# Performance work log

Hardware: AMD Instinct MI355X
Metric: run time of the kernel (lower is better)

Reference implementation:

```python
import jax, jax.numpy as jnp
import numpy as np

N_QUBITS = 12
N_LAYERS = 3
N_LABELS = 28
LN_EPS = 1e-5

_CNOT = jnp.array([[1, 0, 0, 0],
                   [0, 1, 0, 0],
                   [0, 0, 0, 1],
                   [0, 0, 1, 0]], dtype=jnp.complex64).reshape(2, 2, 2, 2)


def _apply_1q(state, U, wire):
    # state: (2,)*N_QUBITS complex, U: (2,2)
    state = jnp.tensordot(U, state, axes=((1,), (wire,)))
    return jnp.moveaxis(state, 0, wire)


def _apply_cnot(state, ctrl, tgt):
    state = jnp.tensordot(_CNOT, state, axes=((2, 3), (ctrl, tgt)))
    return jnp.moveaxis(state, (0, 1), (ctrl, tgt))


def _ry(theta):
    c = jnp.cos(theta / 2).astype(jnp.complex64)
    s = jnp.sin(theta / 2).astype(jnp.complex64)
    return jnp.array([[c, -s], [s, c]])


def _rot(phi, theta, omega):
    # PennyLane Rot(phi, theta, omega) = RZ(omega) RY(theta) RZ(phi)
    c = jnp.cos(theta / 2)
    s = jnp.sin(theta / 2)
    ep = jnp.exp(-0.5j * (phi + omega))
    em = jnp.exp(-0.5j * (phi - omega))
    return jnp.array([[ep * c, -jnp.conj(em) * s],
                      [em * s, jnp.conj(ep) * c]]).astype(jnp.complex64)


def _circuit(angles, weights):
    # angles: (N_QUBITS,), weights: (N_LAYERS, N_QUBITS, 3)
    state = jnp.zeros((2,) * N_QUBITS, dtype=jnp.complex64)
    state = state.at[(0,) * N_QUBITS].set(1.0)
    # AngleEmbedding, rotation='Y'
    for w in range(N_QUBITS):
        state = _apply_1q(state, _ry(angles[w]), w)
    # StronglyEntanglingLayers: Rot on each wire then CNOT ring with range r
    for l in range(N_LAYERS):
        for w in range(N_QUBITS):
            state = _apply_1q(state, _rot(weights[l, w, 0], weights[l, w, 1], weights[l, w, 2]), w)
        r = (l % (N_QUBITS - 1)) + 1
        for w in range(N_QUBITS):
            state = _apply_cnot(state, w, (w + r) % N_QUBITS)
    probs = jnp.real(state * jnp.conj(state))
    zs = []
    for w in range(N_QUBITS):
        p = jnp.sum(probs, axis=tuple(i for i in range(N_QUBITS) if i != w))
        zs.append(p[0] - p[1])
    return jnp.stack(zs)


def setup_inputs() -> dict:
    key = jax.random.key(0)
    ks = jax.random.split(key, 10)
    B = 512
    d_in = 768
    return {
        "x": jax.random.normal(ks[0], (B, d_in), dtype=jnp.float32),
        "proj_w": jax.random.normal(ks[1], (N_QUBITS, d_in), dtype=jnp.float32) * (1.0 / np.sqrt(d_in)),
        "proj_b": jnp.zeros((N_QUBITS,), dtype=jnp.float32),
        "ln_w": jnp.ones((N_QUBITS,), dtype=jnp.float32),
        "ln_b": jnp.zeros((N_QUBITS,), dtype=jnp.float32),
        "q_w": jax.random.uniform(ks[2], (N_LAYERS, N_QUBITS, 3), dtype=jnp.float32) * 2 * np.pi,
        "h1_w": jax.random.normal(ks[3], (256, N_QUBITS), dtype=jnp.float32) * (1.0 / np.sqrt(N_QUBITS)),
        "h1_b": jnp.zeros((256,), dtype=jnp.float32),
        "h2_w": jax.random.normal(ks[4], (N_LABELS, 256), dtype=jnp.float32) * (1.0 / np.sqrt(256)),
        "h2_b": jnp.zeros((N_LABELS,), dtype=jnp.float32),
    }


def reference(x, proj_w, proj_b, ln_w, ln_b, q_w, h1_w, h1_b, h2_w, h2_b):
    h = jnp.tanh(x @ proj_w.T + proj_b)                       # (B, 12)
    mu = jnp.mean(h, axis=-1, keepdims=True)
    var = jnp.mean((h - mu) ** 2, axis=-1, keepdims=True)
    hn = (h - mu) / jnp.sqrt(var + LN_EPS) * ln_w + ln_b      # LayerNorm(12)
    q = jax.vmap(_circuit, in_axes=(0, None))(hn, q_w)        # (B, 12) PauliZ expvals
    z = jax.nn.relu(q @ h1_w.T + h1_b)                        # Dropout is identity in eval
    return z @ h2_w.T + h2_b                                  # (B, 28)
```

## Files before the change

kernel.cpp:

```cpp
#include <hip/hip_runtime.h>
#include <math.h>

#define D_IN 768
#define NLAB 28

struct Map { int rb[2]; int lb[6]; int wb[4]; };
constexpr Map MP[4] = {
    {{10, 11}, {4, 5, 6, 7, 8, 9}, {0, 1, 2, 3}},
    {{0, 1}, {2, 3, 8, 9, 10, 11}, {4, 5, 6, 7}},
    {{6, 7}, {5, 4, 2, 3, 0, 1}, {8, 9, 10, 11}},
    {{0, 1}, {2, 3, 8, 9, 10, 11}, {4, 5, 6, 7}},
};
constexpr int regPos(int e, int b) { for (int k = 0; k < 2; ++k) if (MP[e].rb[k] == b) return k; return -1; }
constexpr int lanePos(int e, int b) { for (int j = 0; j < 6; ++j) if (MP[e].lb[j] == b) return j; return -1; }
constexpr int wavePos(int e, int b) { for (int m = 0; m < 4; ++m) if (MP[e].wb[m] == b) return m; return -1; }

constexpr int stateOf(int e, int wv, int lane, int r) {
    int i = 0;
    for (int k = 0; k < 2; ++k) i |= ((r >> k) & 1) << MP[e].rb[k];
    for (int j = 0; j < 6; ++j) i |= ((lane >> j) & 1) << MP[e].lb[j];
    for (int m = 0; m < 4; ++m) i |= ((wv >> m) & 1) << MP[e].wb[m];
    return i;
}
constexpr int slotOf(int e, int i) {
    int r = 0, ln = 0, wv = 0;
    for (int k = 0; k < 2; ++k) r |= ((i >> MP[e].rb[k]) & 1) << k;
    for (int j = 0; j < 6; ++j) ln |= ((i >> MP[e].lb[j]) & 1) << j;
    for (int m = 0; m < 4; ++m) wv |= ((i >> MP[e].wb[m]) & 1) << m;
    return (wv << 8) | (ln << 2) | r;
}
constexpr int swzl(int s) { return s ^ (((s >> 4) ^ (s >> 8)) & 15); }

template <int J>
__device__ __forceinline__ float lx(float v) {
    if constexpr (J == 0 || J == 1 || J == 3) {
        constexpr int ctrl = (J == 0) ? 0xB1 : (J == 1) ? 0x4E : 0x128;
        return __int_as_float(__builtin_amdgcn_update_dpp(
            0, __float_as_int(v), ctrl, 0xF, 0xF, true));
    } else if constexpr (J == 2 || J == 4) {
        constexpr int off = (J == 2) ? 0x101F : 0x401F;
        return __int_as_float(__builtin_amdgcn_ds_swizzle(__float_as_int(v), off));
    } else {
        return __shfl_xor(v, 32, 64);
    }
}
__device__ __forceinline__ float waveRed(float v) {
    v += lx<0>(v); v += lx<1>(v); v += lx<2>(v);
    v += lx<3>(v); v += lx<4>(v); v += lx<5>(v);
    return v;
}

struct CU2 { float2 rr, im; };
struct G4 { CU2 u00, u01, u10, u11; };

__device__ __forceinline__ float2 cmul(const CU2 u, const float2 a) {
    float2 t;
    asm("v_pk_mul_f32 %0, %1, %2 op_sel:[0,1] op_sel_hi:[1,0]"
        : "=v"(t) : "v"(u.im), "v"(a));
    asm("v_pk_fma_f32 %0, %1, %2, %3"
        : "=v"(t) : "v"(u.rr), "v"(a), "v"(t));
    return t;
}
__device__ __forceinline__ float2 cfma(const CU2 u, const float2 a, float2 acc) {
    asm("v_pk_fma_f32 %0, %1, %2, %3 op_sel:[0,1,0] op_sel_hi:[1,0,1]"
        : "=v"(acc) : "v"(u.im), "v"(a), "v"(acc));
    asm("v_pk_fma_f32 %0, %1, %2, %3"
        : "=v"(acc) : "v"(u.rr), "v"(a), "v"(acc));
    return acc;
}

template <int E, int B>
__device__ __forceinline__ void rotg(float2 (&a)[4], int lane, const G4& gg) {
    const G4 g = gg;
    constexpr int k = regPos(E, B);
    if constexpr (k >= 0) {
        constexpr int m = 1 << k;
#pragma unroll
        for (int r = 0; r < 4; ++r)
            if (!(r & m)) {
                const float2 a0 = a[r], a1 = a[r | m];
                a[r]     = cfma(g.u01, a1, cmul(g.u00, a0));
                a[r | m] = cfma(g.u10, a0, cmul(g.u11, a1));
            }
    } else {
        constexpr int j = lanePos(E, B);
        static_assert(j >= 0, "rot on wave bit");
        const bool hi = (lane >> j) & 1;
        CU2 co, cp;
        co.rr = hi ? g.u11.rr : g.u00.rr;  co.im = hi ? g.u11.im : g.u00.im;
        cp.rr = hi ? g.u10.rr : g.u01.rr;  cp.im = hi ? g.u10.im : g.u01.im;
#pragma unroll
        for (int r = 0; r < 4; ++r) {
            float2 p;
            p.x = lx<j>(a[r].x);
            p.y = lx<j>(a[r].y);
            a[r] = cfma(cp, p, cmul(co, a[r]));
        }
    }
}

template <int E, int C, int T>
__device__ __forceinline__ void cnot(float2 (&a)[4], int lane, int wv) {
    constexpr int kc = regPos(E, C), jc = lanePos(E, C), mc = wavePos(E, C);
    constexpr int kt = regPos(E, T), jt = lanePos(E, T);
    static_assert(wavePos(E, T) < 0, "cnot target on wave bit");
    if constexpr (kt >= 0) {
        constexpr int mt = 1 << kt;
        if constexpr (kc >= 0) {
            constexpr int mcb = 1 << kc;
#pragma unroll
            for (int r = 0; r < 4; ++r)
                if ((r & mcb) && !(r & mt)) { float2 t = a[r]; a[r] = a[r | mt]; a[r | mt] = t; }
        } else if constexpr (jc >= 0) {
            const bool p = (lane >> jc) & 1;
#pragma unroll
            for (int r = 0; r < 4; ++r)
                if (!(r & mt)) {
                    const float2 lo = a[r], hi = a[r | mt];
                    a[r].x = p ? hi.x : lo.x;       a[r].y = p ? hi.y : lo.y;
                    a[r | mt].x = p ? lo.x : hi.x;  a[r | mt].y = p ? lo.y : hi.y;
                }
        } else {
            if ((wv >> mc) & 1) {
#pragma unroll
                for (int r = 0; r < 4; ++r)
                    if (!(r & mt)) { float2 t = a[r]; a[r] = a[r | mt]; a[r | mt] = t; }
            }
        }
    } else {
        if constexpr (kc >= 0) {
            constexpr int mcb = 1 << kc;
#pragma unroll
            for (int r = 0; r < 4; ++r)
                if (r & mcb) { a[r].x = lx<jt>(a[r].x); a[r].y = lx<jt>(a[r].y); }
        } else if constexpr (jc >= 0) {
            const bool p = (lane >> jc) & 1;
#pragma unroll
            for (int r = 0; r < 4; ++r) {
                const float px = lx<jt>(a[r].x), py = lx<jt>(a[r].y);
                a[r].x = p ? px : a[r].x;  a[r].y = p ? py : a[r].y;
            }
        } else {
            if ((wv >> mc) & 1) {
#pragma unroll
                for (int r = 0; r < 4; ++r) { a[r].x = lx<jt>(a[r].x); a[r].y = lx<jt>(a[r].y); }
            }
        }
    }
}

template <int PE, int CE>
__device__ __forceinline__ void remap(float2 (&a)[4], int lane, int wv, float2* st) {
    const int wbase = swzl((wv << 8) | (lane << 2));
#pragma unroll
    for (int r = 0; r < 4; ++r) st[wbase ^ r] = a[r];
    __syncthreads();
    const int rbase = swzl(slotOf(PE, stateOf(CE, wv, lane, 0)));
#pragma unroll
    for (int r = 0; r < 4; ++r) {
        const int d = swzl(slotOf(PE, stateOf(CE, 0, 0, r)));
        a[r] = st[rbase ^ d];
    }
    __syncthreads();
}

constexpr int MASKW[12] = {0x124, 0x092, 0x049, 0x900, 0x480, 0x240,
                           0x920, 0x490, 0x248, 0x924, 0x492, 0x249};
constexpr int rmOf(int w) { int v = 0; for (int k = 0; k < 2; ++k) v |= ((MASKW[w] >> MP[3].rb[k]) & 1) << k; return v; }
constexpr int lmOf(int w) { int v = 0; for (int j = 0; j < 6; ++j) v |= ((MASKW[w] >> MP[3].lb[j]) & 1) << j; return v; }
constexpr int wmOf(int w) { int v = 0; for (int m = 0; m < 4; ++m) v |= ((MASKW[w] >> MP[3].wb[m]) & 1) << m; return v; }
constexpr int RMa[12] = {rmOf(0),rmOf(1),rmOf(2),rmOf(3),rmOf(4),rmOf(5),rmOf(6),rmOf(7),rmOf(8),rmOf(9),rmOf(10),rmOf(11)};
constexpr int LMa[12] = {lmOf(0),lmOf(1),lmOf(2),lmOf(3),lmOf(4),lmOf(5),lmOf(6),lmOf(7),lmOf(8),lmOf(9),lmOf(10),lmOf(11)};
constexpr int WMa[12] = {wmOf(0),wmOf(1),wmOf(2),wmOf(3),wmOf(4),wmOf(5),wmOf(6),wmOf(7),wmOf(8),wmOf(9),wmOf(10),wmOf(11)};

__global__ __launch_bounds__(1024, 8) void hybrid_r6(
    const float* __restrict__ x, const float* __restrict__ proj_w,
    const float* __restrict__ proj_b, const float* __restrict__ ln_w,
    const float* __restrict__ ln_b, const float* __restrict__ q_w,
    const float* __restrict__ h1_w, const float* __restrict__ h1_b,
    const float* __restrict__ h2_w, const float* __restrict__ h2_b,
    float* __restrict__ out) {
    __shared__ float2 st[4096];
    __shared__ G4 rotU[36];
    __shared__ float hbuf[12];
    __shared__ float red[12 * 16];
    __shared__ float z1[256];
    __shared__ float qz[12];

    const int b = blockIdx.x;
    const int tid = threadIdx.x;
    const int lane = tid & 63;
    const int wv = tid >> 6;

    if (wv < 12) {
        const float* xr = x + (size_t)b * D_IN;
        const float* wr = proj_w + wv * D_IN;
        float s = 0.f;
#pragma unroll
        for (int k = 0; k < 12; ++k) s += xr[lane + k * 64] * wr[lane + k * 64];
        s = waveRed(s);
        if (lane == 0) hbuf[wv] = tanhf(s + proj_b[wv]);
    }
    __syncthreads();

    if (tid < 36) {
        const float phi = q_w[3 * tid], th = q_w[3 * tid + 1], om = q_w[3 * tid + 2];
        float sth, cth, sa, ca, sb, cb;
        sincosf(0.5f * th, &sth, &cth);
        sincosf(0.5f * (phi + om), &sa, &ca);
        sincosf(0.5f * (phi - om), &sb, &cb);
        float R0r = cth * ca, R0i = -cth * sa;
        float R1r = -sth * cb, R1i = -sth * sb;
        float R2r = sth * cb, R2i = -sth * sb;
        float R3r = cth * ca, R3i = cth * sa;
        if (tid < 12) {
            float mu = 0.f;
#pragma unroll
            for (int k = 0; k < 12; ++k) mu += hbuf[k];
            mu *= (1.f / 12.f);
            float var = 0.f;
#pragma unroll
            for (int k = 0; k < 12; ++k) { const float d = hbuf[k] - mu; var += d * d; }
            var *= (1.f / 12.f);
            const float inv = 1.f / sqrtf(var + 1e-5f);
            const float ang = (hbuf[tid] - mu) * inv * ln_w[tid] + ln_b[tid];
            float sy, cy;
            sincosf(0.5f * ang, &sy, &cy);
            const float M0r = R0r * cy + R1r * sy, M0i = R0i * cy + R1i * sy;
            const float M1r = -R0r * sy + R1r * cy, M1i = -R0i * sy + R1i * cy;
            const float M2r = R2r * cy + R3r * sy, M2i = R2i * cy + R3i * sy;
            const float M3r = -R2r * sy + R3r * cy, M3i = -R2i * sy + R3i * cy;
            R0r = M0r; R0i = M0i; R1r = M1r; R1i = M1i;
            R2r = M2r; R2i = M2i; R3r = M3r; R3i = M3i;
        }
        G4 g;
        g.u00.rr = make_float2(R0r, R0r); g.u00.im = make_float2(-R0i, R0i);
        g.u01.rr = make_float2(R1r, R1r); g.u01.im = make_float2(-R1i, R1i);
        g.u10.rr = make_float2(R2r, R2r); g.u10.im = make_float2(-R2i, R2i);
        g.u11.rr = make_float2(R3r, R3r); g.u11.im = make_float2(-R3i, R3i);
        rotU[tid] = g;
    }
    __syncthreads();

    float2 a[4];
#pragma unroll
    for (int r = 0; r < 4; ++r) a[r] = make_float2(0.f, 0.f);
    if (tid == 0) a[0].x = 1.f;

    rotg<0, 11>(a, lane, rotU[0]); rotg<0, 10>(a, lane, rotU[1]); rotg<0, 9>(a, lane, rotU[2]);
    rotg<0, 8>(a, lane, rotU[3]);  rotg<0, 7>(a, lane, rotU[4]);  rotg<0, 6>(a, lane, rotU[5]);
    rotg<0, 5>(a, lane, rotU[6]);  rotg<0, 4>(a, lane, rotU[7]);
    cnot<0, 11, 10>(a, lane, wv); cnot<0, 10, 9>(a, lane, wv); cnot<0, 9, 8>(a, lane, wv);
    cnot<0, 8, 7>(a, lane, wv);   cnot<0, 7, 6>(a, lane, wv);  cnot<0, 6, 5>(a, lane, wv);
    cnot<0, 5, 4>(a, lane, wv);
    remap<0, 1>(a, lane, wv, st);
    rotg<1, 3>(a, lane, rotU[8]); rotg<1, 2>(a, lane, rotU[9]);
    rotg<1, 1>(a, lane, rotU[10]); rotg<1, 0>(a, lane, rotU[11]);
    cnot<1, 4, 3>(a, lane, wv); cnot<1, 3, 2>(a, lane, wv); cnot<1, 2, 1>(a, lane, wv);
    cnot<1, 1, 0>(a, lane, wv); cnot<1, 0, 11>(a, lane, wv);
    rotg<1, 11>(a, lane, rotU[12]); rotg<1, 10>(a, lane, rotU[13]);
    rotg<1, 9>(a, lane, rotU[14]);  rotg<1, 8>(a, lane, rotU[15]);
    rotg<1, 3>(a, lane, rotU[20]);  rotg<1, 2>(a, lane, rotU[21]);
    rotg<1, 1>(a, lane, rotU[22]);  rotg<1, 0>(a, lane, rotU[23]);
    cnot<1, 11, 9>(a, lane, wv); cnot<1, 10, 8>(a, lane, wv);
    remap<1, 2>(a, lane, wv, st);
    rotg<2, 7>(a, lane, rotU[16]); rotg<2, 6>(a, lane, rotU[17]);
    rotg<2, 5>(a, lane, rotU[18]); rotg<2, 4>(a, lane, rotU[19]);
    cnot<2, 9, 7>(a, lane, wv); cnot<2, 8, 6>(a, lane, wv); cnot<2, 7, 5>(a, lane, wv);
    cnot<2, 6, 4>(a, lane, wv); cnot<2, 5, 3>(a, lane, wv); cnot<2, 4, 2>(a, lane, wv);
    cnot<2, 3, 1>(a, lane, wv); cnot<2, 2, 0>(a, lane, wv);
    rotg<2, 7>(a, lane, rotU[28]); rotg<2, 6>(a, lane, rotU[29]);
    rotg<2, 5>(a, lane, rotU[30]); rotg<2, 4>(a, lane, rotU[31]);
    rotg<2, 3>(a, lane, rotU[32]); rotg<2, 2>(a, lane, rotU[33]);
    remap<2, 3>(a, lane, wv, st);
    cnot<3, 1, 11>(a, lane, wv); cnot<3, 0, 10>(a, lane, wv);
    rotg<3, 11>(a, lane, rotU[24]); rotg<3, 10>(a, lane, rotU[25]);
    rotg<3, 9>(a, lane, rotU[26]);  rotg<3, 8>(a, lane, rotU[27]);
    rotg<3, 1>(a, lane, rotU[34]);  rotg<3, 0>(a, lane, rotU[35]);

    {
        const float p0 = a[0].x * a[0].x + a[0].y * a[0].y;
        const float p1 = a[1].x * a[1].x + a[1].y * a[1].y;
        const float p2 = a[2].x * a[2].x + a[2].y * a[2].y;
        const float p3 = a[3].x * a[3].x + a[3].y * a[3].y;
        const float s[4] = {p0 + p1 + p2 + p3, p0 - p1 + p2 - p3,
                            p0 + p1 - p2 - p3, p0 - p1 - p2 + p3};
#pragma unroll
        for (int w = 0; w < 12; ++w) {
            const int sgn = (__popc(lane & LMa[w]) + __popc(wv & WMa[w])) & 1;
            float v = sgn ? -s[RMa[w]] : s[RMa[w]];
            v = waveRed(v);
            if (lane == 0) red[w * 16 + wv] = v;
        }
    }
    __syncthreads();
    if (tid < 12) {
        float q = 0.f;
#pragma unroll
        for (int m = 0; m < 16; ++m) q += red[tid * 16 + m];
        qz[tid] = q;
    }
    __syncthreads();

    if (tid < 256) {
        float s = h1_b[tid];
#pragma unroll
        for (int k = 0; k < 12; ++k) s += qz[k] * h1_w[tid * 12 + k];
        z1[tid] = fmaxf(s, 0.f);
    }
    __syncthreads();

    if (wv < 14) {
#pragma unroll
        for (int jj = 0; jj < 2; ++jj) {
            const int j = wv * 2 + jj;
            const float* wr = h2_w + j * 256;
            float s = 0.f;
#pragma unroll
            for (int k = 0; k < 4; ++k) s += z1[lane + k * 64] * wr[lane + k * 64];
            s = waveRed(s);
            if (lane == 0) out[(size_t)b * NLAB + j] = s + h2_b[j];
        }
    }
}

extern "C" void kernel_launch(void* const* d_in, const int* in_sizes, int n_in,
                              void* d_out, int out_size, void* d_ws, size_t ws_size,
                              hipStream_t stream) {
    const float* x      = (const float*)d_in[0];
    const float* proj_w = (const float*)d_in[1];
    const float* proj_b = (const float*)d_in[2];
    const float* ln_w   = (const float*)d_in[3];
    const float* ln_b   = (const float*)d_in[4];
    const float* q_w    = (const float*)d_in[5];
    const float* h1_w   = (const float*)d_in[6];
    const float* h1_b   = (const float*)d_in[7];
    const float* h2_w   = (const float*)d_in[8];
    const float* h2_b   = (const float*)d_in[9];
    float* out = (float*)d_out;

    const int B = in_sizes[0] / D_IN;
    hybrid_r6<<<dim3(B), dim3(1024), 0, stream>>>(x, proj_w, proj_b, ln_w, ln_b,
                                                  q_w, h1_w, h1_b, h2_w, h2_b, out);
}
```

Baseline: 32.93 us.

## Split gate preparation into a separate kernel and read gates as scalar operands

```diff
diff --git a/kernel.cpp b/kernel.cpp
--- a/kernel.cpp
+++ b/kernel.cpp
@@ -53,7 +53,22 @@
 struct CU2 { float2 rr, im; };
 struct G4 { CU2 u00, u01, u10, u11; };
 
-__device__ __forceinline__ float2 cmul(const CU2 u, const float2 a) {
+__device__ __forceinline__ float2 cmuls(const CU2 u, const float2 a) {
+    float2 t;
+    asm("v_pk_mul_f32 %0, %1, %2 op_sel:[0,1] op_sel_hi:[1,0]"
+        : "=v"(t) : "s"(u.im), "v"(a));
+    asm("v_pk_fma_f32 %0, %1, %2, %3"
+        : "=v"(t) : "s"(u.rr), "v"(a), "v"(t));
+    return t;
+}
+__device__ __forceinline__ float2 cfmas(const CU2 u, const float2 a, float2 acc) {
+    asm("v_pk_fma_f32 %0, %1, %2, %3 op_sel:[0,1,0] op_sel_hi:[1,0,1]"
+        : "=v"(acc) : "s"(u.im), "v"(a), "v"(acc));
+    asm("v_pk_fma_f32 %0, %1, %2, %3"
+        : "=v"(acc) : "s"(u.rr), "v"(a), "v"(acc));
+    return acc;
+}
+__device__ __forceinline__ float2 cmulv(const CU2 u, const float2 a) {
     float2 t;
     asm("v_pk_mul_f32 %0, %1, %2 op_sel:[0,1] op_sel_hi:[1,0]"
         : "=v"(t) : "v"(u.im), "v"(a));
@@ -61,7 +76,7 @@
         : "=v"(t) : "v"(u.rr), "v"(a), "v"(t));
     return t;
 }
-__device__ __forceinline__ float2 cfma(const CU2 u, const float2 a, float2 acc) {
+__device__ __forceinline__ float2 cfmav(const CU2 u, const float2 a, float2 acc) {
     asm("v_pk_fma_f32 %0, %1, %2, %3 op_sel:[0,1,0] op_sel_hi:[1,0,1]"
         : "=v"(acc) : "v"(u.im), "v"(a), "v"(acc));
     asm("v_pk_fma_f32 %0, %1, %2, %3"
@@ -70,8 +85,8 @@
 }
 
 template <int E, int B>
-__device__ __forceinline__ void rotg(float2 (&a)[4], int lane, const G4& gg) {
-    const G4 g = gg;
+__device__ __forceinline__ void rotg(float2 (&a)[4], int lane, const G4* __restrict__ gp) {
+    const G4 g = *gp;
     constexpr int k = regPos(E, B);
     if constexpr (k >= 0) {
         constexpr int m = 1 << k;
@@ -79,8 +94,8 @@
         for (int r = 0; r < 4; ++r)
             if (!(r & m)) {
                 const float2 a0 = a[r], a1 = a[r | m];
-                a[r]     = cfma(g.u01, a1, cmul(g.u00, a0));
-                a[r | m] = cfma(g.u10, a0, cmul(g.u11, a1));
+                a[r]     = cfmas(g.u01, a1, cmuls(g.u00, a0));
+                a[r | m] = cfmas(g.u10, a0, cmuls(g.u11, a1));
             }
     } else {
         constexpr int j = lanePos(E, B);
@@ -94,7 +109,7 @@
             float2 p;
             p.x = lx<j>(a[r].x);
             p.y = lx<j>(a[r].y);
-            a[r] = cfma(cp, p, cmul(co, a[r]));
+            a[r] = cfmav(cp, p, cmulv(co, a[r]));
         }
     }
 }
@@ -173,37 +188,36 @@
 constexpr int LMa[12] = {lmOf(0),lmOf(1),lmOf(2),lmOf(3),lmOf(4),lmOf(5),lmOf(6),lmOf(7),lmOf(8),lmOf(9),lmOf(10),lmOf(11)};
 constexpr int WMa[12] = {wmOf(0),wmOf(1),wmOf(2),wmOf(3),wmOf(4),wmOf(5),wmOf(6),wmOf(7),wmOf(8),wmOf(9),wmOf(10),wmOf(11)};
 
-__global__ __launch_bounds__(1024, 8) void hybrid_r6(
+__global__ __launch_bounds__(256) void prep_gates(
     const float* __restrict__ x, const float* __restrict__ proj_w,
     const float* __restrict__ proj_b, const float* __restrict__ ln_w,
     const float* __restrict__ ln_b, const float* __restrict__ q_w,
-    const float* __restrict__ h1_w, const float* __restrict__ h1_b,
-    const float* __restrict__ h2_w, const float* __restrict__ h2_b,
-    float* __restrict__ out) {
-    __shared__ float2 st[4096];
-    __shared__ G4 rotU[36];
+    G4* __restrict__ wsF, G4* __restrict__ wsS) {
     __shared__ float hbuf[12];
-    __shared__ float red[12 * 16];
-    __shared__ float z1[256];
-    __shared__ float qz[12];
-
     const int b = blockIdx.x;
     const int tid = threadIdx.x;
     const int lane = tid & 63;
     const int wv = tid >> 6;
 
-    if (wv < 12) {
+    {
         const float* xr = x + (size_t)b * D_IN;
-        const float* wr = proj_w + wv * D_IN;
-        float s = 0.f;
-#pragma unroll
-        for (int k = 0; k < 12; ++k) s += xr[lane + k * 64] * wr[lane + k * 64];
-        s = waveRed(s);
-        if (lane == 0) hbuf[wv] = tanhf(s + proj_b[wv]);
-    }
-    __syncthreads();
-
-    if (tid < 36) {
+        float xv[12];
+#pragma unroll
+        for (int k = 0; k < 12; ++k) xv[k] = xr[lane + k * 64];
+#pragma unroll
+        for (int jj = 0; jj < 3; ++jj) {
+            const int j = wv * 3 + jj;
+            const float* wr = proj_w + j * D_IN;
+            float s = 0.f;
+#pragma unroll
+            for (int k = 0; k < 12; ++k) s += xv[k] * wr[lane + k * 64];
+            s = waveRed(s);
+            if (lane == 0) hbuf[j] = tanhf(s + proj_b[j]);
+        }
+    }
+    __syncthreads();
+
+    if (tid < 36 && (tid < 12 || b == 0)) {
         const float phi = q_w[3 * tid], th = q_w[3 * tid + 1], om = q_w[3 * tid + 2];
         float sth, cth, sa, ca, sb, cb;
         sincosf(0.5f * th, &sth, &cth);
@@ -238,45 +252,62 @@
         g.u01.rr = make_float2(R1r, R1r); g.u01.im = make_float2(-R1i, R1i);
         g.u10.rr = make_float2(R2r, R2r); g.u10.im = make_float2(-R2i, R2i);
         g.u11.rr = make_float2(R3r, R3r); g.u11.im = make_float2(-R3i, R3i);
-        rotU[tid] = g;
-    }
-    __syncthreads();
+        G4* dst = (tid < 12) ? (wsF + (size_t)b * 12 + tid) : (wsS + (tid - 12));
+        *dst = g;
+    }
+}
+
+__global__ __launch_bounds__(1024, 8) void hybrid_r7(
+    const float* __restrict__ h1_w, const float* __restrict__ h1_b,
+    const float* __restrict__ h2_w, const float* __restrict__ h2_b,
+    const G4* __restrict__ wsF, const G4* __restrict__ wsS,
+    float* __restrict__ out) {
+    __shared__ float2 st[4096];
+    __shared__ float red[12 * 16];
+    __shared__ float z1[256];
+    __shared__ float qz[12];
+
+    const int b = blockIdx.x;
+    const int tid = threadIdx.x;
+    const int lane = tid & 63;
+    const int wv = tid >> 6;
+    const G4* __restrict__ gF = wsF + (size_t)b * 12;
 
     float2 a[4];
 #pragma unroll
     for (int r = 0; r < 4; ++r) a[r] = make_float2(0.f, 0.f);
     if (tid == 0) a[0].x = 1.f;
 
-    rotg<0, 11>(a, lane, rotU[0]); rotg<0, 10>(a, lane, rotU[1]); rotg<0, 9>(a, lane, rotU[2]);
-    rotg<0, 8>(a, lane, rotU[3]);  rotg<0, 7>(a, lane, rotU[4]);  rotg<0, 6>(a, lane, rotU[5]);
-    rotg<0, 5>(a, lane, rotU[6]);  rotg<0, 4>(a, lane, rotU[7]);
+    rotg<0, 11>(a, lane, gF + 0); rotg<0, 10>(a, lane, gF + 1); rotg<0, 9>(a, lane, gF + 2);
+    rotg<0, 8>(a, lane, gF + 3);  rotg<0, 7>(a, lane, gF + 4);  rotg<0, 6>(a, lane, gF + 5);
+    rotg<0, 5>(a, lane, gF + 6);  rotg<0, 4>(a, lane, gF + 7);
     cnot<0, 11, 10>(a, lane, wv); cnot<0, 10, 9>(a, lane, wv); cnot<0, 9, 8>(a, lane, wv);
     cnot<0, 8, 7>(a, lane, wv);   cnot<0, 7, 6>(a, lane, wv);  cnot<0, 6, 5>(a, lane, wv);
     cnot<0, 5, 4>(a, lane, wv);
     remap<0, 1>(a, lane, wv, st);
-    rotg<1, 3>(a, lane, rotU[8]); rotg<1, 2>(a, lane, rotU[9]);
-    rotg<1, 1>(a, lane, rotU[10]); rotg<1, 0>(a, lane, rotU[11]);
+    rotg<1, 3>(a, lane, gF + 8);  rotg<1, 2>(a, lane, gF + 9);
+    rotg<1, 1>(a, lane, gF + 10); rotg<1, 0>(a, lane, gF + 11);
     cnot<1, 4, 3>(a, lane, wv); cnot<1, 3, 2>(a, lane, wv); cnot<1, 2, 1>(a, lane, wv);
     cnot<1, 1, 0>(a, lane, wv); cnot<1, 0, 11>(a, lane, wv);
-    rotg<1, 11>(a, lane, rotU[12]); rotg<1, 10>(a, lane, rotU[13]);
-    rotg<1, 9>(a, lane, rotU[14]);  rotg<1, 8>(a, lane, rotU[15]);
-    rotg<1, 3>(a, lane, rotU[20]);  rotg<1, 2>(a, lane, rotU[21]);
-    rotg<1, 1>(a, lane, rotU[22]);  rotg<1, 0>(a, lane, rotU[23]);
+    rotg<1, 11>(a, lane, wsS + 0); rotg<1, 10>(a, lane, wsS + 1);
+    rotg<1, 9>(a, lane, wsS + 2);  rotg<1, 8>(a, lane, wsS + 3);
+    rotg<1, 3>(a, lane, wsS + 8);  rotg<1, 2>(a, lane, wsS + 9);
+    rotg<1, 1>(a, lane, wsS + 10); rotg<1, 0>(a, lane, wsS + 11);
     cnot<1, 11, 9>(a, lane, wv); cnot<1, 10, 8>(a, lane, wv);
     remap<1, 2>(a, lane, wv, st);
-    rotg<2, 7>(a, lane, rotU[16]); rotg<2, 6>(a, lane, rotU[17]);
-    rotg<2, 5>(a, lane, rotU[18]); rotg<2, 4>(a, lane, rotU[19]);
+    rotg<2, 7>(a, lane, wsS + 4); rotg<2, 6>(a, lane, wsS + 5);
+    rotg<2, 5>(a, lane, wsS + 6); rotg<2, 4>(a, lane, wsS + 7);
     cnot<2, 9, 7>(a, lane, wv); cnot<2, 8, 6>(a, lane, wv); cnot<2, 7, 5>(a, lane, wv);
     cnot<2, 6, 4>(a, lane, wv); cnot<2, 5, 3>(a, lane, wv); cnot<2, 4, 2>(a, lane, wv);
     cnot<2, 3, 1>(a, lane, wv); cnot<2, 2, 0>(a, lane, wv);
-    rotg<2, 7>(a, lane, rotU[28]); rotg<2, 6>(a, lane, rotU[29]);
-    rotg<2, 5>(a, lane, rotU[30]); rotg<2, 4>(a, lane, rotU[31]);
-    rotg<2, 3>(a, lane, rotU[32]); rotg<2, 2>(a, lane, rotU[33]);
+    rotg<2, 7>(a, lane, wsS + 16); rotg<2, 6>(a, lane, wsS + 17);
+    rotg<2, 5>(a, lane, wsS + 18); rotg<2, 4>(a, lane, wsS + 19);
+    rotg<2, 3>(a, lane, wsS + 20); rotg<2, 2>(a, lane, wsS + 21);
     remap<2, 3>(a, lane, wv, st);
     cnot<3, 1, 11>(a, lane, wv); cnot<3, 0, 10>(a, lane, wv);
-    rotg<3, 11>(a, lane, rotU[24]); rotg<3, 10>(a, lane, rotU[25]);
-    rotg<3, 9>(a, lane, rotU[26]);  rotg<3, 8>(a, lane, rotU[27]);
-    rotg<3, 1>(a, lane, rotU[34]);  rotg<3, 0>(a, lane, rotU[35]);
+    rotg<3, 11>(a, lane, wsS + 12); rotg<3, 10>(a, lane, wsS + 13);
+    rotg<3, 9>(a, lane, wsS + 14);  rotg<3, 8>(a, lane, wsS + 15);
+    rotg<3, 1>(a, lane, wsS + 22);  rotg<3, 0>(a, lane, wsS + 23);
 
     {
         const float p0 = a[0].x * a[0].x + a[0].y * a[0].y;
@@ -340,6 +371,11 @@
     float* out = (float*)d_out;
 
     const int B = in_sizes[0] / D_IN;
-    hybrid_r6<<<dim3(B), dim3(1024), 0, stream>>>(x, proj_w, proj_b, ln_w, ln_b,
-                                                  q_w, h1_w, h1_b, h2_w, h2_b, out);
-}
+    G4* wsF = (G4*)d_ws;
+    G4* wsS = wsF + (size_t)B * 12;
+
+    prep_gates<<<dim3(B), dim3(256), 0, stream>>>(x, proj_w, proj_b, ln_w, ln_b,
+                                                  q_w, wsF, wsS);
+    hybrid_r7<<<dim3(B), dim3(1024), 0, stream>>>(h1_w, h1_b, h2_w, h2_b,
+                                                  wsF, wsS, out);
+}
```

After: 37.74 us. +14.6%, slower.

## Double-buffer remap scratch, overlap gate build, swap swizzles for DPP/permlane

Applied to the files above, without the earlier changes.

```diff
diff --git a/kernel.cpp b/kernel.cpp
--- a/kernel.cpp
+++ b/kernel.cpp
@@ -37,11 +37,26 @@
         constexpr int ctrl = (J == 0) ? 0xB1 : (J == 1) ? 0x4E : 0x128;
         return __int_as_float(__builtin_amdgcn_update_dpp(
             0, __float_as_int(v), ctrl, 0xF, 0xF, true));
-    } else if constexpr (J == 2 || J == 4) {
-        constexpr int off = (J == 2) ? 0x101F : 0x401F;
-        return __int_as_float(__builtin_amdgcn_ds_swizzle(__float_as_int(v), off));
+    } else if constexpr (J == 2) {
+        const float tshl = __int_as_float(__builtin_amdgcn_update_dpp(
+            0, __float_as_int(v), 0x104, 0xF, 0xF, true));
+        const float tshr = __int_as_float(__builtin_amdgcn_update_dpp(
+            0, __float_as_int(v), 0x114, 0xF, 0xF, true));
+        return (threadIdx.x & 4) ? tshr : tshl;
+    } else if constexpr (J == 4) {
+#if __has_builtin(__builtin_amdgcn_permlane16_swap)
+        auto pr = __builtin_amdgcn_permlane16_swap(__float_as_int(v), __float_as_int(v), false, false);
+        return (__int_as_float((int)pr[0]) + __int_as_float((int)pr[1])) - v;
+#else
+        return __int_as_float(__builtin_amdgcn_ds_swizzle(__float_as_int(v), 0x401F));
+#endif
     } else {
+#if __has_builtin(__builtin_amdgcn_permlane32_swap)
+        auto pr = __builtin_amdgcn_permlane32_swap(__float_as_int(v), __float_as_int(v), false, false);
+        return (__int_as_float((int)pr[0]) + __int_as_float((int)pr[1])) - v;
+#else
         return __shfl_xor(v, 32, 64);
+#endif
     }
 }
 __device__ __forceinline__ float waveRed(float v) {
@@ -53,7 +68,7 @@
 struct CU2 { float2 rr, im; };
 struct G4 { CU2 u00, u01, u10, u11; };
 
-__device__ __forceinline__ float2 cmul(const CU2 u, const float2 a) {
+__device__ __forceinline__ float2 cmulv(const CU2 u, const float2 a) {
     float2 t;
     asm("v_pk_mul_f32 %0, %1, %2 op_sel:[0,1] op_sel_hi:[1,0]"
         : "=v"(t) : "v"(u.im), "v"(a));
@@ -61,7 +76,7 @@
         : "=v"(t) : "v"(u.rr), "v"(a), "v"(t));
     return t;
 }
-__device__ __forceinline__ float2 cfma(const CU2 u, const float2 a, float2 acc) {
+__device__ __forceinline__ float2 cfmav(const CU2 u, const float2 a, float2 acc) {
     asm("v_pk_fma_f32 %0, %1, %2, %3 op_sel:[0,1,0] op_sel_hi:[1,0,1]"
         : "=v"(acc) : "v"(u.im), "v"(a), "v"(acc));
     asm("v_pk_fma_f32 %0, %1, %2, %3"
@@ -79,8 +94,8 @@
         for (int r = 0; r < 4; ++r)
             if (!(r & m)) {
                 const float2 a0 = a[r], a1 = a[r | m];
-                a[r]     = cfma(g.u01, a1, cmul(g.u00, a0));
-                a[r | m] = cfma(g.u10, a0, cmul(g.u11, a1));
+                a[r]     = cfmav(g.u01, a1, cmulv(g.u00, a0));
+                a[r | m] = cfmav(g.u10, a0, cmulv(g.u11, a1));
             }
     } else {
         constexpr int j = lanePos(E, B);
@@ -94,7 +109,7 @@
             float2 p;
             p.x = lx<j>(a[r].x);
             p.y = lx<j>(a[r].y);
-            a[r] = cfma(cp, p, cmul(co, a[r]));
+            a[r] = cfmav(cp, p, cmulv(co, a[r]));
         }
     }
 }
@@ -161,7 +176,6 @@
         const int d = swzl(slotOf(PE, stateOf(CE, 0, 0, r)));
         a[r] = st[rbase ^ d];
     }
-    __syncthreads();
 }
 
 constexpr int MASKW[12] = {0x124, 0x092, 0x049, 0x900, 0x480, 0x240,
@@ -173,14 +187,34 @@
 constexpr int LMa[12] = {lmOf(0),lmOf(1),lmOf(2),lmOf(3),lmOf(4),lmOf(5),lmOf(6),lmOf(7),lmOf(8),lmOf(9),lmOf(10),lmOf(11)};
 constexpr int WMa[12] = {wmOf(0),wmOf(1),wmOf(2),wmOf(3),wmOf(4),wmOf(5),wmOf(6),wmOf(7),wmOf(8),wmOf(9),wmOf(10),wmOf(11)};
 
-__global__ __launch_bounds__(1024, 8) void hybrid_r6(
+__device__ __forceinline__ void buildRot(int g, const float* __restrict__ q_w, float R[8]) {
+    const float phi = q_w[3 * g], th = q_w[3 * g + 1], om = q_w[3 * g + 2];
+    float sth, cth, sa, ca, sb, cb;
+    sincosf(0.5f * th, &sth, &cth);
+    sincosf(0.5f * (phi + om), &sa, &ca);
+    sincosf(0.5f * (phi - om), &sb, &cb);
+    R[0] = cth * ca;  R[1] = -cth * sa;
+    R[2] = -sth * cb; R[3] = -sth * sb;
+    R[4] = sth * cb;  R[5] = -sth * sb;
+    R[6] = cth * ca;  R[7] = cth * sa;
+}
+__device__ __forceinline__ void storeGate(G4* dst, const float R[8]) {
+    G4 g;
+    g.u00.rr = make_float2(R[0], R[0]); g.u00.im = make_float2(-R[1], R[1]);
+    g.u01.rr = make_float2(R[2], R[2]); g.u01.im = make_float2(-R[3], R[3]);
+    g.u10.rr = make_float2(R[4], R[4]); g.u10.im = make_float2(-R[5], R[5]);
+    g.u11.rr = make_float2(R[6], R[6]); g.u11.im = make_float2(-R[7], R[7]);
+    *dst = g;
+}
+
+__global__ __launch_bounds__(1024, 8) void hybrid_r9(
     const float* __restrict__ x, const float* __restrict__ proj_w,
     const float* __restrict__ proj_b, const float* __restrict__ ln_w,
     const float* __restrict__ ln_b, const float* __restrict__ q_w,
     const float* __restrict__ h1_w, const float* __restrict__ h1_b,
     const float* __restrict__ h2_w, const float* __restrict__ h2_b,
     float* __restrict__ out) {
-    __shared__ float2 st[4096];
+    __shared__ float2 st[2][4096];
     __shared__ G4 rotU[36];
     __shared__ float hbuf[12];
     __shared__ float red[12 * 16];
@@ -201,44 +235,35 @@
         s = waveRed(s);
         if (lane == 0) hbuf[wv] = tanhf(s + proj_b[wv]);
     }
-    __syncthreads();
-
-    if (tid < 36) {
-        const float phi = q_w[3 * tid], th = q_w[3 * tid + 1], om = q_w[3 * tid + 2];
-        float sth, cth, sa, ca, sb, cb;
-        sincosf(0.5f * th, &sth, &cth);
-        sincosf(0.5f * (phi + om), &sa, &ca);
-        sincosf(0.5f * (phi - om), &sb, &cb);
-        float R0r = cth * ca, R0i = -cth * sa;
-        float R1r = -sth * cb, R1i = -sth * sb;
-        float R2r = sth * cb, R2i = -sth * sb;
-        float R3r = cth * ca, R3i = cth * sa;
-        if (tid < 12) {
-            float mu = 0.f;
-#pragma unroll
-            for (int k = 0; k < 12; ++k) mu += hbuf[k];
-            mu *= (1.f / 12.f);
-            float var = 0.f;
-#pragma unroll
-            for (int k = 0; k < 12; ++k) { const float d = hbuf[k] - mu; var += d * d; }
-            var *= (1.f / 12.f);
-            const float inv = 1.f / sqrtf(var + 1e-5f);
-            const float ang = (hbuf[tid] - mu) * inv * ln_w[tid] + ln_b[tid];
-            float sy, cy;
-            sincosf(0.5f * ang, &sy, &cy);
-            const float M0r = R0r * cy + R1r * sy, M0i = R0i * cy + R1i * sy;
-            const float M1r = -R0r * sy + R1r * cy, M1i = -R0i * sy + R1i * cy;
-            const float M2r = R2r * cy + R3r * sy, M2i = R2i * cy + R3i * sy;
-            const float M3r = -R2r * sy + R3r * cy, M3i = -R2i * sy + R3i * cy;
-            R0r = M0r; R0i = M0i; R1r = M1r; R1i = M1i;
-            R2r = M2r; R2i = M2i; R3r = M3r; R3i = M3i;
-        }
-        G4 g;
-        g.u00.rr = make_float2(R0r, R0r); g.u00.im = make_float2(-R0i, R0i);
-        g.u01.rr = make_float2(R1r, R1r); g.u01.im = make_float2(-R1i, R1i);
-        g.u10.rr = make_float2(R2r, R2r); g.u10.im = make_float2(-R2i, R2i);
-        g.u11.rr = make_float2(R3r, R3r); g.u11.im = make_float2(-R3i, R3i);
-        rotU[tid] = g;
+    if (tid >= 768 && tid < 792) {
+        const int g = tid - 768 + 12;
+        float R[8];
+        buildRot(g, q_w, R);
+        storeGate(&rotU[g], R);
+    }
+    __syncthreads();
+
+    if (lane == 0 && wv < 12) {
+        float mu = 0.f;
+#pragma unroll
+        for (int k = 0; k < 12; ++k) mu += hbuf[k];
+        mu *= (1.f / 12.f);
+        float var = 0.f;
+#pragma unroll
+        for (int k = 0; k < 12; ++k) { const float d = hbuf[k] - mu; var += d * d; }
+        var *= (1.f / 12.f);
+        const float inv = 1.f / sqrtf(var + 1e-5f);
+        const float ang = (hbuf[wv] - mu) * inv * ln_w[wv] + ln_b[wv];
+        float sy, cy;
+        sincosf(0.5f * ang, &sy, &cy);
+        float R[8];
+        buildRot(wv, q_w, R);
+        float M[8];
+        M[0] = R[0] * cy + R[2] * sy;  M[1] = R[1] * cy + R[3] * sy;
+        M[2] = -R[0] * sy + R[2] * cy; M[3] = -R[1] * sy + R[3] * cy;
+        M[4] = R[4] * cy + R[6] * sy;  M[5] = R[5] * cy + R[7] * sy;
+        M[6] = -R[4] * sy + R[6] * cy; M[7] = -R[5] * sy + R[7] * cy;
+        storeGate(&rotU[wv], M);
     }
     __syncthreads();
 
@@ -253,7 +278,7 @@
     cnot<0, 11, 10>(a, lane, wv); cnot<0, 10, 9>(a, lane, wv); cnot<0, 9, 8>(a, lane, wv);
     cnot<0, 8, 7>(a, lane, wv);   cnot<0, 7, 6>(a, lane, wv);  cnot<0, 6, 5>(a, lane, wv);
     cnot<0, 5, 4>(a, lane, wv);
-    remap<0, 1>(a, lane, wv, st);
+    remap<0, 1>(a, lane, wv, st[0]);
     rotg<1, 3>(a, lane, rotU[8]); rotg<1, 2>(a, lane, rotU[9]);
     rotg<1, 1>(a, lane, rotU[10]); rotg<1, 0>(a, lane, rotU[11]);
     cnot<1, 4, 3>(a, lane, wv); cnot<1, 3, 2>(a, lane, wv); cnot<1, 2, 1>(a, lane, wv);
@@ -263,7 +288,7 @@
     rotg<1, 3>(a, lane, rotU[20]);  rotg<1, 2>(a, lane, rotU[21]);
     rotg<1, 1>(a, lane, rotU[22]);  rotg<1, 0>(a, lane, rotU[23]);
     cnot<1, 11, 9>(a, lane, wv); cnot<1, 10, 8>(a, lane, wv);
-    remap<1, 2>(a, lane, wv, st);
+    remap<1, 2>(a, lane, wv, st[1]);
     rotg<2, 7>(a, lane, rotU[16]); rotg<2, 6>(a, lane, rotU[17]);
     rotg<2, 5>(a, lane, rotU[18]); rotg<2, 4>(a, lane, rotU[19]);
     cnot<2, 9, 7>(a, lane, wv); cnot<2, 8, 6>(a, lane, wv); cnot<2, 7, 5>(a, lane, wv);
@@ -272,7 +297,7 @@
     rotg<2, 7>(a, lane, rotU[28]); rotg<2, 6>(a, lane, rotU[29]);
     rotg<2, 5>(a, lane, rotU[30]); rotg<2, 4>(a, lane, rotU[31]);
     rotg<2, 3>(a, lane, rotU[32]); rotg<2, 2>(a, lane, rotU[33]);
-    remap<2, 3>(a, lane, wv, st);
+    remap<2, 3>(a, lane, wv, st[0]);
     cnot<3, 1, 11>(a, lane, wv); cnot<3, 0, 10>(a, lane, wv);
     rotg<3, 11>(a, lane, rotU[24]); rotg<3, 10>(a, lane, rotU[25]);
     rotg<3, 9>(a, lane, rotU[26]);  rotg<3, 8>(a, lane, rotU[27]);
@@ -340,6 +365,6 @@
     float* out = (float*)d_out;
 
     const int B = in_sizes[0] / D_IN;
-    hybrid_r6<<<dim3(B), dim3(1024), 0, stream>>>(x, proj_w, proj_b, ln_w, ln_b,
+    hybrid_r9<<<dim3(B), dim3(1024), 0, stream>>>(x, proj_w, proj_b, ln_w, ln_b,
                                                   q_w, h1_w, h1_b, h2_w, h2_b, out);
 }
```

After: 40.99 us. +24.5%, slower.
